# Kernel tuning notes

Measured on AMD Instinct MI355X. Metric: run time of the kernel, lower is better.

Reference implementation:

```python
import jax, jax.numpy as jnp
import numpy as np

# PairwiseChannelAdd(aggregation='max', mode='off-diag', source_axis=1)
# For each source channel k in [0, C-2]:
#   right = x[:, k+1:] + x[:, k];  left = x[:, :k+1] + x[:, k]
#   union of right+left covers ALL j in [0, C-1] (diagonal j==k included via `left`).
#   connec_k = max over (pair axis j, time axis T) of (x[:, j] + x[:, k])  -> [B, 1, F]
# stack over k -> [C-1, B, 1, F]; transpose([1,2,0,3]) -> [B, 1, C-1, F]

B, C, T, F = 8, 160, 512, 32

def setup_inputs() -> dict:
    key = jax.random.key(0)
    x = jax.random.normal(key, (B, C, T, F), dtype=jnp.float32)
    return {"x": x}

def reference(x):
    c = x.shape[1]
    ks = jnp.arange(c - 1)
    # lax.map keeps memory at one [B,C,T,F] pairwise-sum intermediate per step
    def per_k(k):
        # x[:, k] -> [B, T, F]; broadcast-add against all channels j -> [B, C, T, F]
        s = x + x[:, k][:, None, :, :]
        return jnp.max(s, axis=(1, 2))  # reduce over pair (j) and time -> [B, F]
    out = jax.lax.map(per_k, ks)        # [C-1, B, F]
    return jnp.transpose(out, (1, 0, 2))[:, None, :, :]  # [B, 1, C-1, F]
```

## Files before the change

kernel.cpp:

```cpp
#include <hip/hip_runtime.h>
#include <math.h>

#define B_DIM 8
#define C_DIM 160
#define T_DIM 512
#define F_DIM 32
#define F4 (F_DIM / 4)

__device__ __forceinline__ float4 fmax4(float4 a, float4 b) {
    return make_float4(fmaxf(a.x, b.x), fmaxf(a.y, b.y),
                       fmaxf(a.z, b.z), fmaxf(a.w, b.w));
}
__device__ __forceinline__ float4 fadd4(float4 a, float4 b) {
    return make_float4(a.x + b.x, a.y + b.y, a.z + b.z, a.w + b.w);
}

__global__ __launch_bounds__(256)
void channel_max_kernel(const float* __restrict__ x, float* __restrict__ M) {
    const int bt = blockIdx.x;
    const int b = bt >> 9;
    const int t = bt & (T_DIM - 1);
    const int tid = threadIdx.x;
    const int f4 = tid & (F4 - 1);
    const int c0 = tid >> 3;

    const float4* __restrict__ x4 = (const float4*)x;
    float4 acc = make_float4(-INFINITY, -INFINITY, -INFINITY, -INFINITY);
    #pragma unroll
    for (int c = c0; c < C_DIM; c += 32) {
        float4 v = x4[((b * C_DIM + c) * T_DIM + t) * F4 + f4];
        acc = fmax4(acc, v);
    }

    __shared__ float4 red[256];
    red[tid] = acc;
    __syncthreads();
    #pragma unroll
    for (int s = 128; s >= F4; s >>= 1) {
        if (tid < s) red[tid] = fmax4(red[tid], red[tid + s]);
        __syncthreads();
    }
    if (tid < F4) {
        ((float4*)M)[bt * F4 + tid] = red[tid];
    }
}

__global__ __launch_bounds__(256)
void pair_out_kernel(const float* __restrict__ x, const float* __restrict__ M,
                     float* __restrict__ out) {
    const int bk = blockIdx.x;
    const int b = bk / (C_DIM - 1);
    const int k = bk - b * (C_DIM - 1);
    const int tid = threadIdx.x;
    const int f4 = tid & (F4 - 1);
    const int t0 = tid >> 3;

    const float4* __restrict__ xk = (const float4*)x + (b * C_DIM + k) * T_DIM * F4;
    const float4* __restrict__ Mb = (const float4*)M + b * T_DIM * F4;

    float4 acc = make_float4(-INFINITY, -INFINITY, -INFINITY, -INFINITY);
    #pragma unroll 4
    for (int t = t0; t < T_DIM; t += 32) {
        float4 v = xk[t * F4 + f4];
        float4 m = Mb[t * F4 + f4];
        acc = fmax4(acc, fadd4(v, m));
    }

    __shared__ float4 red[256];
    red[tid] = acc;
    __syncthreads();
    #pragma unroll
    for (int s = 128; s >= F4; s >>= 1) {
        if (tid < s) red[tid] = fmax4(red[tid], red[tid + s]);
        __syncthreads();
    }
    if (tid < F4) {
        ((float4*)out)[bk * F4 + tid] = red[tid];
    }
}

extern "C" void kernel_launch(void* const* d_in, const int* in_sizes, int n_in,
                              void* d_out, int out_size, void* d_ws, size_t ws_size,
                              hipStream_t stream) {
    const float* x = (const float*)d_in[0];
    float* out = (float*)d_out;
    float* M = (float*)d_ws;

    channel_max_kernel<<<B_DIM * T_DIM, 256, 0, stream>>>(x, M);
    pair_out_kernel<<<B_DIM * (C_DIM - 1), 256, 0, stream>>>(x, M, out);
}
```

Baseline: 130.8 us.

## Restructure both kernels: multi-timestep blocks and single-wave shuffle reduction

The channel-max kernel now handles 8 timesteps per block, with 4 channel slices per block, and replaces the long shared-memory tree with two steps. The pair kernel uses one 64-lane wave per (b,k), streams the contiguous T*F slab, and reduces with xor shuffles instead of shared memory and barriers. The aim is to cut block count, barrier overhead and launch granularity so both kernels run closer to memory bandwidth. Using fewer, smaller blocks may lower occupancy and the memory parallelism it provides.

```diff
diff --git a/kernel.cpp b/kernel.cpp
--- a/kernel.cpp
+++ b/kernel.cpp
@@ -6,6 +6,7 @@
 #define T_DIM 512
 #define F_DIM 32
 #define F4 (F_DIM / 4)
+#define C1 (C_DIM - 1)
 
 __device__ __forceinline__ float4 fmax4(float4 a, float4 b) {
     return make_float4(fmaxf(a.x, b.x), fmaxf(a.y, b.y),
@@ -14,68 +15,66 @@
 __device__ __forceinline__ float4 fadd4(float4 a, float4 b) {
     return make_float4(a.x + b.x, a.y + b.y, a.z + b.z, a.w + b.w);
 }
+__device__ __forceinline__ float4 shfl_xor4(float4 v, int m) {
+    return make_float4(__shfl_xor(v.x, m), __shfl_xor(v.y, m),
+                       __shfl_xor(v.z, m), __shfl_xor(v.w, m));
+}
 
 __global__ __launch_bounds__(256)
 void channel_max_kernel(const float* __restrict__ x, float* __restrict__ M) {
-    const int bt = blockIdx.x;
-    const int b = bt >> 9;
-    const int t = bt & (T_DIM - 1);
+    const int bt8 = blockIdx.x;
+    const int b = bt8 >> 6;
+    const int t_base = (bt8 & 63) << 3;
     const int tid = threadIdx.x;
-    const int f4 = tid & (F4 - 1);
-    const int c0 = tid >> 3;
+    const int f4 = tid & 7;
+    const int tl = (tid >> 3) & 7;
+    const int cs = tid >> 6;
+    const int t = t_base + tl;
 
     const float4* __restrict__ x4 = (const float4*)x;
+    const int base = (b * C_DIM * T_DIM + t) * F4 + f4;
+
     float4 acc = make_float4(-INFINITY, -INFINITY, -INFINITY, -INFINITY);
-    #pragma unroll
-    for (int c = c0; c < C_DIM; c += 32) {
-        float4 v = x4[((b * C_DIM + c) * T_DIM + t) * F4 + f4];
-        acc = fmax4(acc, v);
+    #pragma unroll 8
+    for (int i = 0; i < 40; ++i) {
+        const int c = i * 4 + cs;
+        acc = fmax4(acc, x4[base + c * (T_DIM * F4)]);
     }
 
     __shared__ float4 red[256];
     red[tid] = acc;
     __syncthreads();
-    #pragma unroll
-    for (int s = 128; s >= F4; s >>= 1) {
-        if (tid < s) red[tid] = fmax4(red[tid], red[tid + s]);
-        __syncthreads();
-    }
-    if (tid < F4) {
-        ((float4*)M)[bt * F4 + tid] = red[tid];
+    if (tid < 128) red[tid] = fmax4(red[tid], red[tid + 128]);
+    __syncthreads();
+    if (tid < 64) {
+        const float4 v = fmax4(red[tid], red[tid + 64]);
+        ((float4*)M)[(b * T_DIM + t_base) * F4 + tid] = v;
     }
 }
 
-__global__ __launch_bounds__(256)
+__global__ __launch_bounds__(64)
 void pair_out_kernel(const float* __restrict__ x, const float* __restrict__ M,
                      float* __restrict__ out) {
     const int bk = blockIdx.x;
-    const int b = bk / (C_DIM - 1);
-    const int k = bk - b * (C_DIM - 1);
-    const int tid = threadIdx.x;
-    const int f4 = tid & (F4 - 1);
-    const int t0 = tid >> 3;
+    const int b = bk / C1;
+    const int k = bk - b * C1;
+    const int lane = threadIdx.x;
 
-    const float4* __restrict__ xk = (const float4*)x + (b * C_DIM + k) * T_DIM * F4;
-    const float4* __restrict__ Mb = (const float4*)M + b * T_DIM * F4;
+    const float4* __restrict__ xk = (const float4*)x + (b * C_DIM + k) * (T_DIM * F4);
+    const float4* __restrict__ Mb = (const float4*)M + b * (T_DIM * F4);
 
     float4 acc = make_float4(-INFINITY, -INFINITY, -INFINITY, -INFINITY);
-    #pragma unroll 4
-    for (int t = t0; t < T_DIM; t += 32) {
-        float4 v = xk[t * F4 + f4];
-        float4 m = Mb[t * F4 + f4];
-        acc = fmax4(acc, fadd4(v, m));
+    #pragma unroll 8
+    for (int j = 0; j < T_DIM * F4 / 64; ++j) {
+        const int idx = j * 64 + lane;
+        acc = fmax4(acc, fadd4(xk[idx], Mb[idx]));
     }
 
-    __shared__ float4 red[256];
-    red[tid] = acc;
-    __syncthreads();
-    #pragma unroll
-    for (int s = 128; s >= F4; s >>= 1) {
-        if (tid < s) red[tid] = fmax4(red[tid], red[tid + s]);
-        __syncthreads();
-    }
-    if (tid < F4) {
-        ((float4*)out)[bk * F4 + tid] = red[tid];
+    acc = fmax4(acc, shfl_xor4(acc, 8));
+    acc = fmax4(acc, shfl_xor4(acc, 16));
+    acc = fmax4(acc, shfl_xor4(acc, 32));
+    if (lane < 8) {
+        ((float4*)out)[bk * F4 + lane] = acc;
     }
 }
 
@@ -86,6 +85,6 @@
     float* out = (float*)d_out;
     float* M = (float*)d_ws;
 
-    channel_max_kernel<<<B_DIM * T_DIM, 256, 0, stream>>>(x, M);
-    pair_out_kernel<<<B_DIM * (C_DIM - 1), 256, 0, stream>>>(x, M, out);
+    channel_max_kernel<<<B_DIM * (T_DIM / 8), 256, 0, stream>>>(x, M);
+    pair_out_kernel<<<B_DIM * C1, 64, 0, stream>>>(x, M, out);
 }
```

Result: faster. 127.1 us (-2.9%).
